# Kernel tuning notes

Measured on AMD Instinct MI355X. Metric: run time of the kernel, lower is better.

The kernel has to match this reference:

```python
import jax, jax.numpy as jnp
import numpy as np


def setup_inputs() -> dict:
    key = jax.random.key(0)
    k1, k2, k3, k4 = jax.random.split(key, 4)
    B, To, Tw, D = 64, 36, 32, 512  # Bo == Bw == B required by .diag()
    o = jax.random.normal(k1, (B, To, D), dtype=jnp.float32)
    u = jax.random.normal(k2, (B, To, D), dtype=jnp.float32)
    w = jax.random.normal(k3, (B, Tw, D), dtype=jnp.float32)
    mask = jax.random.randint(k4, (B, Tw), 0, 2).astype(jnp.int32)  # 1 = masked
    return {"o": o, "u": u, "w": w, "mask": mask}


def reference(o, u, w, mask):
    # o: (Bo, To, D) contextualized object feats; u: (Bo, To, D) uncontextualized;
    # w: (Bw, Tw, D) caption word feats; mask: (Bw, Tw) with 1 = padded word.
    D = w.shape[-1]
    # Original computes sum(Kw * Ku, 4) over a broadcast (Bw,Bo,Tw,To,D) tensor;
    # that is exactly a cross-batch contraction -> einsum.
    scores = jnp.einsum('wtd,bod->wbto', w, u) / jnp.sqrt(jnp.asarray(D, jnp.float32))
    att = jax.nn.softmax(scores, axis=3)              # softmax over objects To
    att_V_o = jnp.einsum('wbto,bod->wbtd', att, o)    # attention-weighted objects
    logits = jnp.einsum('wbtd,wtd->wbt', att_V_o, w)  # (Bw, Bo, Tw)
    log_sm = jax.nn.log_softmax(logits, axis=1)       # InfoNCE over Bo
    keep = 1.0 - mask.astype(log_sm.dtype)            # (Bw, Tw), 1 = valid word
    log_sm = log_sm * keep[:, None, :]
    num_non_mask = jnp.sum(keep, axis=1)[:, None, None]  # (Bw, 1, 1)
    log_sm = log_sm / (num_non_mask + 1e-6)
    loss_mat = jnp.sum(log_sm, axis=2)                # (Bw, Bo)
    loss = -jnp.mean(jnp.diagonal(loss_mat))
    return (loss, att, att_V_o)
```

## Files before the change

### kernel.cpp

```cpp
#include <hip/hip_runtime.h>

#define BB 64
#define TO 36
#define TW 32
#define DD 512

typedef short short8 __attribute__((ext_vector_type(8)));
typedef float floatx4 __attribute__((ext_vector_type(4)));


__device__ __forceinline__ unsigned short f2bf(float f) {
  unsigned int x = __builtin_bit_cast(unsigned int, f);
  x += 0x7FFFu + ((x >> 16) & 1u);
  return (unsigned short)(x >> 16);
}

__device__ __forceinline__ short8 ld8(const unsigned short* p) {
  return __builtin_bit_cast(short8, *(const uint4*)p);
}

__global__ __launch_bounds__(256) void prep_kernel(
    const float* __restrict__ o_g, const float* __restrict__ u_g,
    const float* __restrict__ w_g, unsigned short* __restrict__ wbf,
    unsigned short* __restrict__ ubf, unsigned short* __restrict__ ot) {
  const int blk = blockIdx.x, tid = threadIdx.x;
  if (blk < 512) {
    int i8 = blk * 256 + tid;
    const float4* src = (const float4*)w_g;
    float4 f0 = src[i8 * 2], f1 = src[i8 * 2 + 1];
    uint4 d;
    d.x = (unsigned)f2bf(f0.x) | ((unsigned)f2bf(f0.y) << 16);
    d.y = (unsigned)f2bf(f0.z) | ((unsigned)f2bf(f0.w) << 16);
    d.z = (unsigned)f2bf(f1.x) | ((unsigned)f2bf(f1.y) << 16);
    d.w = (unsigned)f2bf(f1.z) | ((unsigned)f2bf(f1.w) << 16);
    ((uint4*)wbf)[i8] = d;
  } else if (blk < 1088) {
    int i8 = (blk - 512) * 256 + tid;
    const float4* src = (const float4*)u_g;
    float4 f0 = src[i8 * 2], f1 = src[i8 * 2 + 1];
    uint4 d;
    d.x = (unsigned)f2bf(f0.x) | ((unsigned)f2bf(f0.y) << 16);
    d.y = (unsigned)f2bf(f0.z) | ((unsigned)f2bf(f0.w) << 16);
    d.z = (unsigned)f2bf(f1.x) | ((unsigned)f2bf(f1.y) << 16);
    d.w = (unsigned)f2bf(f1.z) | ((unsigned)f2bf(f1.w) << 16);
    ((uint4*)ubf)[i8] = d;
  } else {
    int t2 = (blk - 1088) * 256 + tid;
    int b = t2 >> 9, d = t2 & 511;
    uint4 bufv[8];
    unsigned short* buf = (unsigned short*)bufv;
#pragma unroll
    for (int o = 0; o < 64; ++o)
      buf[o] = (o < TO) ? f2bf(o_g[((b * TO + o) << 9) + d]) : (unsigned short)0;
    uint4* dst = (uint4*)(ot + ((size_t)((b << 9) + d) << 6));
#pragma unroll
    for (int i = 0; i < 8; ++i) dst[i] = bufv[i];
  }
}

__global__ __launch_bounds__(256) void main_kernel(
    const float* __restrict__ w_g,
    const unsigned short* __restrict__ wbf,
    const unsigned short* __restrict__ ubf,
    const unsigned short* __restrict__ ot,
    float* __restrict__ logits_ws,
    float* __restrict__ att_out,
    float* __restrict__ attV_out) {
  const int b = blockIdx.x;
  const int wv = threadIdx.x >> 6;
  const int wb = blockIdx.y * 4 + wv;
  const int lane = threadIdx.x & 63;
  const int c = lane & 15;
  const int q = lane >> 4;

  __shared__ unsigned short att_s[4][TW][72];
  {
    unsigned int* p = (unsigned int*)&att_s[wv][0][0];
#pragma unroll
    for (int i = 0; i < 18; ++i) p[lane + 64 * i] = 0u;
  }

  const unsigned short* wbp = wbf + (size_t)wb * TW * DD;
  const unsigned short* ubp = ubf + (size_t)b * TO * DD;

  floatx4 acc[2][3];
#pragma unroll
  for (int i = 0; i < 2; ++i)
#pragma unroll
    for (int j = 0; j < 3; ++j) acc[i][j] = (floatx4){0.f, 0.f, 0.f, 0.f};

  int r2 = 32 + c; if (r2 > 35) r2 = 35;
#pragma unroll 2
  for (int kk = 0; kk < 16; ++kk) {
    int k0 = kk * 32 + q * 8;
    short8 a0 = ld8(wbp + c * DD + k0);
    short8 a1 = ld8(wbp + (16 + c) * DD + k0);
    short8 u0 = ld8(ubp + c * DD + k0);
    short8 u1 = ld8(ubp + (16 + c) * DD + k0);
    short8 u2 = ld8(ubp + r2 * DD + k0);
    acc[0][0] = __builtin_amdgcn_mfma_f32_16x16x32_bf16(a0, u0, acc[0][0], 0, 0, 0);
    acc[0][1] = __builtin_amdgcn_mfma_f32_16x16x32_bf16(a0, u1, acc[0][1], 0, 0, 0);
    acc[0][2] = __builtin_amdgcn_mfma_f32_16x16x32_bf16(a0, u2, acc[0][2], 0, 0, 0);
    acc[1][0] = __builtin_amdgcn_mfma_f32_16x16x32_bf16(a1, u0, acc[1][0], 0, 0, 0);
    acc[1][1] = __builtin_amdgcn_mfma_f32_16x16x32_bf16(a1, u1, acc[1][1], 0, 0, 0);
    acc[1][2] = __builtin_amdgcn_mfma_f32_16x16x32_bf16(a1, u2, acc[1][2], 0, 0, 0);
  }

  const float scale = 0.04419417382415922f;
  float attv[2][3][4];
  const bool v2 = (c < 4);
#pragma unroll
  for (int mt = 0; mt < 2; ++mt) {
#pragma unroll
    for (int reg = 0; reg < 4; ++reg) {
      float s0 = acc[mt][0][reg] * scale;
      float s1 = acc[mt][1][reg] * scale;
      float s2 = acc[mt][2][reg] * scale;
      float m = fmaxf(s0, s1);
      if (v2) m = fmaxf(m, s2);
#pragma unroll
      for (int off = 1; off < 16; off <<= 1) m = fmaxf(m, __shfl_xor(m, off));
      float e0 = __expf(s0 - m);
      float e1 = __expf(s1 - m);
      float e2 = v2 ? __expf(s2 - m) : 0.f;
      float sum = e0 + e1 + e2;
#pragma unroll
      for (int off = 1; off < 16; off <<= 1) sum += __shfl_xor(sum, off);
      float inv = 1.f / sum;
      attv[mt][0][reg] = e0 * inv;
      attv[mt][1][reg] = e1 * inv;
      attv[mt][2][reg] = e2 * inv;
    }
  }

  float* attb = att_out + (size_t)(wb * BB + b) * TW * TO;
#pragma unroll
  for (int mt = 0; mt < 2; ++mt)
#pragma unroll
    for (int reg = 0; reg < 4; ++reg) {
      int t = mt * 16 + q * 4 + reg;
#pragma unroll
      for (int nt = 0; nt < 3; ++nt) {
        int oo = nt * 16 + c;
        if (oo < TO) {
          attb[t * TO + oo] = attv[mt][nt][reg];
          att_s[wv][t][oo] = f2bf(attv[mt][nt][reg]);
        }
      }
    }
  __syncthreads();

  short8 a2[2][2];
#pragma unroll
  for (int mt = 0; mt < 2; ++mt)
#pragma unroll
    for (int kk = 0; kk < 2; ++kk)
      a2[mt][kk] = ld8(&att_s[wv][mt * 16 + c][kk * 32 + q * 8]);

  const unsigned short* otp = ot + (size_t)b * DD * 64;
  const float* wrow = w_g + (size_t)wb * TW * DD;
  float* avb = attV_out + (size_t)(wb * BB + b) * TW * DD;
  float lp[2] = {0.f, 0.f};
  float prevA3[2];

  {
    short8 b0 = ld8(otp + c * 64 + q * 8);
    short8 b1 = ld8(otp + c * 64 + 32 + q * 8);
#pragma unroll
    for (int mt = 0; mt < 2; ++mt) {
      floatx4 a = (floatx4){0.f, 0.f, 0.f, 0.f};
      a = __builtin_amdgcn_mfma_f32_16x16x32_bf16(b0, a2[mt][0], a, 0, 0, 0);
      a = __builtin_amdgcn_mfma_f32_16x16x32_bf16(b1, a2[mt][1], a, 0, 0, 0);
      const int t = mt * 16 + c;
      const int dd = q * 4;
      float4 w4 = *(const float4*)&wrow[t * DD + dd];
      lp[mt] += a[0] * w4.x + a[1] * w4.y + a[2] * w4.z + a[3] * w4.w;
      float up = __shfl_up(a[3], 16);
      if (q == 0) {
        avb[t * DD + 0] = a[0];
        avb[t * DD + 1] = a[1];
        avb[t * DD + 2] = a[2];
      } else {
        float4 st = {up, a[0], a[1], a[2]};
        *(float4*)&avb[t * DD + dd - 1] = st;
      }
      prevA3[mt] = a[3];
    }
  }

#pragma unroll 4
  for (int nt2 = 1; nt2 < 32; ++nt2) {
    const int d0 = nt2 * 16;
    short8 b0 = ld8(otp + (d0 + c) * 64 + q * 8);
    short8 b1 = ld8(otp + (d0 + c) * 64 + 32 + q * 8);
#pragma unroll
    for (int mt = 0; mt < 2; ++mt) {
      floatx4 a = (floatx4){0.f, 0.f, 0.f, 0.f};
      a = __builtin_amdgcn_mfma_f32_16x16x32_bf16(b0, a2[mt][0], a, 0, 0, 0);
      a = __builtin_amdgcn_mfma_f32_16x16x32_bf16(b1, a2[mt][1], a, 0, 0, 0);
      const int t = mt * 16 + c;
      const int dd = d0 + q * 4;
      float4 w4 = *(const float4*)&wrow[t * DD + dd];
      lp[mt] += a[0] * w4.x + a[1] * w4.y + a[2] * w4.z + a[3] * w4.w;
      float up = __shfl_up(a[3], 16);
      float carry = __shfl(prevA3[mt], c | 48);
      float first = (q == 0) ? carry : up;
      float4 st = {first, a[0], a[1], a[2]};
      *(float4*)&avb[t * DD + dd - 1] = st;
      prevA3[mt] = a[3];
    }
  }

#pragma unroll
  for (int mt = 0; mt < 2; ++mt) {
    if (q == 3) avb[(mt * 16 + c) * DD + 511] = prevA3[mt];
    float s = lp[mt];
    s += __shfl_xor(s, 16);
    s += __shfl_xor(s, 32);
    if (lane < 16)
      logits_ws[(size_t)(wb * BB + b) * TW + mt * 16 + lane] = s;
  }
}

__global__ __launch_bounds__(64) void loss_kernel(
    const float* __restrict__ logits, const int* __restrict__ mask,
    float* __restrict__ out) {
  int wb = blockIdx.x, lane = threadIdx.x;
  const float* lrow = logits + ((size_t)wb * BB + lane) * TW;
  float accv = 0.f, nnm = 0.f;
  for (int t = 0; t < TW; ++t) {
    float v = lrow[t];
    float m = v;
#pragma unroll
    for (int off = 1; off < 64; off <<= 1) m = fmaxf(m, __shfl_xor(m, off));
    float e = __expf(v - m);
    float s = e;
#pragma unroll
    for (int off = 1; off < 64; off <<= 1) s += __shfl_xor(s, off);
    float diag = __shfl(v, wb);
    float lsm = diag - m - __logf(s);
    float keep = 1.f - (float)mask[wb * TW + t];
    accv += lsm * keep;
    nnm += keep;
  }
  if (lane == 0) atomicAdd(out, -(accv / (nnm + 1e-6f)) * (1.f / 64.f));
}

extern "C" void kernel_launch(void* const* d_in, const int* in_sizes, int n_in,
                              void* d_out, int out_size, void* d_ws, size_t ws_size,
                              hipStream_t stream) {
  const float* o_g = (const float*)d_in[0];
  const float* u_g = (const float*)d_in[1];
  const float* w_g = (const float*)d_in[2];
  const int* mask  = (const int*)d_in[3];

  float* out = (float*)d_out;
  float* att_out  = out + 1;
  float* attV_out = out + 1 + (size_t)BB * BB * TW * TO;

  char* ws = (char*)d_ws;
  unsigned short* wbf = (unsigned short*)(ws + 0);
  unsigned short* ubf = (unsigned short*)(ws + 2097152);
  unsigned short* ot  = (unsigned short*)(ws + 4456448);
  float* logits       = (float*)(ws + 8650752);

  hipMemsetAsync(d_out, 0, sizeof(float), stream);
  prep_kernel<<<1216, 256, 0, stream>>>(o_g, u_g, w_g, wbf, ubf, ot);
  main_kernel<<<dim3(BB, BB / 4), 256, 0, stream>>>(w_g, wbf, ubf, ot, logits,
                                                    att_out, attV_out);
  loss_kernel<<<BB, 64, 0, stream>>>(logits, mask, out);
}
```

Before: 435.3 us.

## Split attention-weighted output across two waves per pair and use nontemporal stores

Each block now handles two word-batches instead of four. Two waves per (wb,b) pair each recompute the scores and softmax redundantly, then each produces one half of the D dimension of att_V_o. Their partial logits are combined through shared memory. Output writes now use nontemporal stores so the large streaming outputs bypass cache. This doubles the wave count on the store-heavy phase to hide latency, at the price of duplicated score/softmax work and an extra block-level sync.

Measured after the change: 413.2 us. 1.05x faster.

```diff
diff --git a/kernel.cpp b/kernel.cpp
--- a/kernel.cpp
+++ b/kernel.cpp
@@ -68,16 +68,24 @@
     float* __restrict__ attV_out) {
   const int b = blockIdx.x;
   const int wv = threadIdx.x >> 6;
-  const int wb = blockIdx.y * 4 + wv;
+  const int sl = wv >> 1;
+  const int dhalf = wv & 1;
+  const int wb = blockIdx.y * 2 + sl;
   const int lane = threadIdx.x & 63;
   const int c = lane & 15;
   const int q = lane >> 4;
 
-  __shared__ unsigned short att_s[4][TW][72];
+  __shared__ unsigned short att_s[2][TW][72];
+  __shared__ float lsum[4][2][16];
+
   {
-    unsigned int* p = (unsigned int*)&att_s[wv][0][0];
-#pragma unroll
-    for (int i = 0; i < 18; ++i) p[lane + 64 * i] = 0u;
+    unsigned int* base = (unsigned int*)&att_s[sl][0][0];
+#pragma unroll
+    for (int i = 0; i < 9; ++i) {
+      int idx = i * 64 + lane;
+      int row = idx / 18, cd = idx - row * 18;
+      base[row * 36 + 18 + cd] = 0u;
+    }
   }
 
   const unsigned short* wbp = wbf + (size_t)wb * TW * DD;
@@ -143,27 +151,28 @@
       for (int nt = 0; nt < 3; ++nt) {
         int oo = nt * 16 + c;
         if (oo < TO) {
-          attb[t * TO + oo] = attv[mt][nt][reg];
-          att_s[wv][t][oo] = f2bf(attv[mt][nt][reg]);
+          if (dhalf == 0)
+            __builtin_nontemporal_store(attv[mt][nt][reg], &attb[t * TO + oo]);
+          att_s[sl][t][oo] = f2bf(attv[mt][nt][reg]);
         }
       }
     }
-  __syncthreads();
 
   short8 a2[2][2];
 #pragma unroll
   for (int mt = 0; mt < 2; ++mt)
 #pragma unroll
     for (int kk = 0; kk < 2; ++kk)
-      a2[mt][kk] = ld8(&att_s[wv][mt * 16 + c][kk * 32 + q * 8]);
+      a2[mt][kk] = ld8(&att_s[sl][mt * 16 + c][kk * 32 + q * 8]);
 
   const unsigned short* otp = ot + (size_t)b * DD * 64;
   const float* wrow = w_g + (size_t)wb * TW * DD;
   float* avb = attV_out + (size_t)(wb * BB + b) * TW * DD;
   float lp[2] = {0.f, 0.f};
   float prevA3[2];
-
-  {
+  int tstart, tend;
+
+  if (dhalf == 0) {
     short8 b0 = ld8(otp + c * 64 + q * 8);
     short8 b1 = ld8(otp + c * 64 + 32 + q * 8);
 #pragma unroll
@@ -177,19 +186,31 @@
       lp[mt] += a[0] * w4.x + a[1] * w4.y + a[2] * w4.z + a[3] * w4.w;
       float up = __shfl_up(a[3], 16);
       if (q == 0) {
-        avb[t * DD + 0] = a[0];
-        avb[t * DD + 1] = a[1];
-        avb[t * DD + 2] = a[2];
+        __builtin_nontemporal_store(a[0], &avb[t * DD + 0]);
+        __builtin_nontemporal_store(a[1], &avb[t * DD + 1]);
+        __builtin_nontemporal_store(a[2], &avb[t * DD + 2]);
       } else {
-        float4 st = {up, a[0], a[1], a[2]};
-        *(float4*)&avb[t * DD + dd - 1] = st;
+        floatx4 st = {up, a[0], a[1], a[2]};
+        __builtin_nontemporal_store(st, (floatx4*)&avb[t * DD + dd - 1]);
       }
       prevA3[mt] = a[3];
     }
+    tstart = 1; tend = 16;
+  } else {
+    short8 b0 = ld8(otp + (240 + c) * 64 + q * 8);
+    short8 b1 = ld8(otp + (240 + c) * 64 + 32 + q * 8);
+#pragma unroll
+    for (int mt = 0; mt < 2; ++mt) {
+      floatx4 a = (floatx4){0.f, 0.f, 0.f, 0.f};
+      a = __builtin_amdgcn_mfma_f32_16x16x32_bf16(b0, a2[mt][0], a, 0, 0, 0);
+      a = __builtin_amdgcn_mfma_f32_16x16x32_bf16(b1, a2[mt][1], a, 0, 0, 0);
+      prevA3[mt] = a[3];
+    }
+    tstart = 16; tend = 32;
   }
 
 #pragma unroll 4
-  for (int nt2 = 1; nt2 < 32; ++nt2) {
+  for (int nt2 = tstart; nt2 < tend; ++nt2) {
     const int d0 = nt2 * 16;
     short8 b0 = ld8(otp + (d0 + c) * 64 + q * 8);
     short8 b1 = ld8(otp + (d0 + c) * 64 + 32 + q * 8);
@@ -205,20 +226,28 @@
       float up = __shfl_up(a[3], 16);
       float carry = __shfl(prevA3[mt], c | 48);
       float first = (q == 0) ? carry : up;
-      float4 st = {first, a[0], a[1], a[2]};
-      *(float4*)&avb[t * DD + dd - 1] = st;
+      floatx4 st = {first, a[0], a[1], a[2]};
+      __builtin_nontemporal_store(st, (floatx4*)&avb[t * DD + dd - 1]);
       prevA3[mt] = a[3];
     }
   }
 
 #pragma unroll
   for (int mt = 0; mt < 2; ++mt) {
-    if (q == 3) avb[(mt * 16 + c) * DD + 511] = prevA3[mt];
+    if (dhalf == 1 && q == 3)
+      __builtin_nontemporal_store(prevA3[mt], &avb[(mt * 16 + c) * DD + 511]);
     float s = lp[mt];
     s += __shfl_xor(s, 16);
     s += __shfl_xor(s, 32);
-    if (lane < 16)
-      logits_ws[(size_t)(wb * BB + b) * TW + mt * 16 + lane] = s;
+    if (lane < 16) lsum[wv][mt][lane] = s;
+  }
+  __syncthreads();
+  if (dhalf == 0 && lane < 16) {
+#pragma unroll
+    for (int mt = 0; mt < 2; ++mt) {
+      float tot = lsum[wv][mt][lane] + lsum[wv + 1][mt][lane];
+      logits_ws[(size_t)(wb * BB + b) * TW + mt * 16 + lane] = tot;
+    }
   }
 }
 
@@ -266,7 +295,7 @@
 
   hipMemsetAsync(d_out, 0, sizeof(float), stream);
   prep_kernel<<<1216, 256, 0, stream>>>(o_g, u_g, w_g, wbf, ubf, ot);
-  main_kernel<<<dim3(BB, BB / 4), 256, 0, stream>>>(w_g, wbf, ubf, ot, logits,
+  main_kernel<<<dim3(BB, BB / 2), 256, 0, stream>>>(w_g, wbf, ubf, ot, logits,
                                                     att_out, attV_out);
   loss_kernel<<<BB, 64, 0, stream>>>(logits, mask, out);
 }
```
